# Kernel optimization log

Measured on AMD Instinct MI355X. Metric: run time of the kernel, lower is better.

The kernel has to match this reference:

```python
import jax, jax.numpy as jnp
import numpy as np

D_MODEL = 256
V_OUT = 256
N1 = 8192
N2 = 8192
NUM_CLASSES = 10


def _cross_sup_con_loss(features, labels_y1, labels_y2):
    """Label-masked softmax contrastive loss over a [N1, N2] score matrix.

    mask[i, j] = 1 if labels_y1[i] == labels_y2[j]. Standard SupCon-style
    stabilized log-softmax over dim 1; loss = -mean_i mean_{j in pos(i)} log p_ij.
    Returns (masked softmax probabilities, scalar loss).
    """
    mask = (labels_y1[:, None] == labels_y2[None, :]).astype(features.dtype)  # [N1, N2]
    logits = features - jax.lax.stop_gradient(jnp.max(features, axis=1, keepdims=True))
    log_prob = logits - jax.nn.logsumexp(logits, axis=1, keepdims=True)  # [N1, N2]
    pos_per_row = jnp.maximum(jnp.sum(mask, axis=1), 1.0)
    mean_log_prob_pos = jnp.sum(mask * log_prob, axis=1) / pos_per_row
    loss = -jnp.mean(mean_log_prob_pos)
    masked_prob = mask * jnp.exp(log_prob)
    return masked_prob, loss


def setup_inputs() -> dict:
    key = jax.random.key(0)
    ks = jax.random.split(key, 10)
    s = 1.0 / np.sqrt(D_MODEL)
    inp = {
        "x1": jax.random.normal(ks[0], (N1, D_MODEL), jnp.float32),
        "x2": jax.random.normal(ks[1], (N2, D_MODEL), jnp.float32),
        "labels_y1": jax.random.randint(ks[2], (N1,), 0, NUM_CLASSES, jnp.int64 if jax.config.jax_enable_x64 else jnp.int32),
        "labels_y2": jax.random.randint(ks[3], (N2,), 0, NUM_CLASSES, jnp.int64 if jax.config.jax_enable_x64 else jnp.int32),
        # Linear params stored as [in, out]; y = x @ W + b
        "Wxq": jax.random.normal(ks[4], (D_MODEL, D_MODEL), jnp.float32) * s,
        "bxq": jnp.zeros((D_MODEL,), jnp.float32),
        "Wxk": jax.random.normal(ks[5], (D_MODEL, D_MODEL), jnp.float32) * s,
        "bxk": jnp.zeros((D_MODEL,), jnp.float32),
        "Wxv": jax.random.normal(ks[6], (D_MODEL, V_OUT), jnp.float32) * s,
        "bxv": jnp.zeros((V_OUT,), jnp.float32),
        "Wout": jax.random.normal(ks[7], (V_OUT, V_OUT), jnp.float32) * s,
        "bout": jnp.zeros((V_OUT,), jnp.float32),
    }
    return inp


def reference(x1, x2, labels_y1, labels_y2, Wxq, bxq, Wxk, bxk, Wxv, bxv, Wout, bout):
    scale = 1.0 / jnp.asarray(D_MODEL, x1.dtype) ** 0.5  # self.d_k overwritten to d_model
    x_q = x1 @ Wxq + bxq                 # [N1, D]
    x_k = x2 @ Wxk + bxk                 # [N2, D]
    x_v = x2 @ Wxv + bxv                 # [N2, V]
    scores = (x_q @ x_k.T) * scale       # [N1, N2]
    masked_prob, loss = _cross_sup_con_loss(scores, labels_y1, labels_y2)
    out = masked_prob @ x_v              # [N1, V]
    res = x1 + out                       # residual (d_model == v_out_dim)
    # F.normalize: L2 along dim=1, eps=1e-12
    norm = jnp.linalg.norm(res, axis=1, keepdims=True)
    res = res / jnp.maximum(norm, 1e-12)
    output = jax.nn.relu(res @ Wout + bout)
    return loss, output
```

## Files before the change

### kernel.cpp

```cpp
#include <hip/hip_runtime.h>
#include <math.h>

#define DM 256
#define NROWS 8192
#define NCOLS 8192
#define LOG2E 1.44269504f
#define LN2F 0.6931471805599453f

typedef __attribute__((ext_vector_type(8)))  __bf16 bf16x8;
typedef __attribute__((ext_vector_type(4)))  __bf16 bf16x4;
typedef __attribute__((ext_vector_type(16))) float  f32x16;

#if __has_builtin(__builtin_amdgcn_exp2f)
#define EXP2F(x) __builtin_amdgcn_exp2f(x)
#else
#define EXP2F(x) exp2f(x)
#endif

__device__ __forceinline__ f32x16 fzero16() {
  f32x16 z;
#pragma unroll
  for (int i = 0; i < 16; ++i) z[i] = 0.f;
  return z;
}

__device__ __forceinline__ void load_lds16(const void* g, void* l) {
  __builtin_amdgcn_global_load_lds(
      (const __attribute__((address_space(1))) unsigned int*)g,
      (__attribute__((address_space(3))) unsigned int*)l, 16, 0, 0);
}

__device__ __forceinline__ bf16x8 cvt8(float4 a, float4 b) {
  bf16x8 v;
  v[0] = (__bf16)a.x; v[1] = (__bf16)a.y; v[2] = (__bf16)a.z; v[3] = (__bf16)a.w;
  v[4] = (__bf16)b.x; v[5] = (__bf16)b.y; v[6] = (__bf16)b.z; v[7] = (__bf16)b.w;
  return v;
}

__device__ __forceinline__ unsigned cvtpk_bf16(float lo, float hi) {
  unsigned r;
  asm("v_cvt_pk_bf16_f32 %0, %1, %2" : "=v"(r) : "v"(lo), "v"(hi));
  return r;
}
__device__ __forceinline__ void swap32(unsigned& a, unsigned& b) {
  asm("v_permlane32_swap_b32 %0, %1" : "+v"(a), "+v"(b));
}

__global__ __launch_bounds__(256) void convert_w_kernel(
    const float* __restrict__ W0, const float* __restrict__ W1,
    const float* __restrict__ W2, const float* __restrict__ W3,
    __bf16* __restrict__ wt) {
  __shared__ float Ls[64][65];
  const int t = threadIdx.x;
  const int mat = blockIdx.x >> 4;
  const int k0 = ((blockIdx.x >> 2) & 3) * 64;
  const int n0 = (blockIdx.x & 3) * 64;
  const float* W = mat == 0 ? W0 : mat == 1 ? W1 : mat == 2 ? W2 : W3;
#pragma unroll
  for (int i = 0; i < 4; ++i) {
    int idx = t + i * 256;
    int row = idx >> 4, c4 = (idx & 15) * 4;
    float4 v = *(const float4*)&W[(size_t)(k0 + row) * DM + n0 + c4];
    Ls[row][c4] = v.x; Ls[row][c4 + 1] = v.y;
    Ls[row][c4 + 2] = v.z; Ls[row][c4 + 3] = v.w;
  }
  __syncthreads();
#pragma unroll
  for (int i = 0; i < 2; ++i) {
    int c = t + i * 256;
    int n = c >> 3, kc = (c & 7) * 8;
    bf16x8 v;
#pragma unroll
    for (int j = 0; j < 8; ++j) v[j] = (__bf16)Ls[kc + j][n];
    *(bf16x8*)&wt[(size_t)mat * 65536 + (size_t)(n0 + n) * DM + k0 + kc] = v;
  }
}

__global__ __launch_bounds__(1024) void hist_kernel(
    const int* __restrict__ lab2, int* __restrict__ counts) {
  __shared__ int h[16];
  const int t = threadIdx.x;
  if (t < 16) h[t] = 0;
  __syncthreads();
  int4 a = *(const int4*)&lab2[t * 8];
  int4 b = *(const int4*)&lab2[t * 8 + 4];
  atomicAdd(&h[a.x & 15], 1); atomicAdd(&h[a.y & 15], 1);
  atomicAdd(&h[a.z & 15], 1); atomicAdd(&h[a.w & 15], 1);
  atomicAdd(&h[b.x & 15], 1); atomicAdd(&h[b.y & 15], 1);
  atomicAdd(&h[b.z & 15], 1); atomicAdd(&h[b.w & 15], 1);
  __syncthreads();
  if (t < 16) counts[t] = h[t];
}

__global__ __launch_bounds__(256) void proj3_kernel(
    const float* __restrict__ x1, const float* __restrict__ x2,
    const __bf16* __restrict__ wt, const float* __restrict__ bxq,
    const float* __restrict__ bxk, const float* __restrict__ bxv,
    __bf16* __restrict__ xqb, __bf16* __restrict__ xkb,
    __bf16* __restrict__ xvT) {
  __shared__ __bf16 W_s[64 * 256];
  const int t = threadIdx.x;
  const int w = t >> 6, l = t & 63, g = l >> 5, l31 = l & 31;
  const int mb = blockIdx.x, nt = blockIdx.y, mat = blockIdx.z;
  const int n0 = nt * 64;
  const float* A = (mat == 0) ? x1 : x2;
  const __bf16* wmat = wt + (size_t)mat * 65536;
  const float* bias = (mat == 0) ? bxq : (mat == 1) ? bxk : bxv;
  const float oscale = (mat == 0) ? (0.0625f * LOG2E) : 1.0f;
#pragma unroll
  for (int o = 0; o < 8; ++o) {
    int cbase = w * 64 + o * 256;
    int chunk = cbase + l;
    int n = chunk >> 5, kb = (chunk & 31) * 16;
    load_lds16((const char*)wmat + (size_t)(n0 + n) * 512 + (kb ^ ((n & 7) << 4)),
               (char*)W_s + (size_t)cbase * 16);
  }
  const int arow = mb * 128 + w * 32 + l31;
  bf16x8 af[16];
#pragma unroll
  for (int ks = 0; ks < 16; ++ks) {
    float4 u0 = *(const float4*)&A[(size_t)arow * DM + ks * 16 + g * 8];
    float4 u1 = *(const float4*)&A[(size_t)arow * DM + ks * 16 + g * 8 + 4];
    af[ks] = cvt8(u0, u1);
  }
  __syncthreads();
  f32x16 acc2[2];
  acc2[0] = fzero16(); acc2[1] = fzero16();
#pragma unroll
  for (int ks = 0; ks < 16; ++ks)
#pragma unroll
    for (int tt = 0; tt < 2; ++tt) {
      int n = tt * 32 + l31;
      bf16x8 b = *(const bf16x8*)&W_s[n * DM + ((ks * 16 + g * 8) ^ ((n & 7) << 3))];
      acc2[tt] = __builtin_amdgcn_mfma_f32_32x32x16_bf16(af[ks], b, acc2[tt], 0, 0, 0);
    }
  const int mrowbase = mb * 128 + w * 32;
#pragma unroll
  for (int tt = 0; tt < 2; ++tt) {
    const int col = n0 + tt * 32 + l31;
    const float bv = bias[col];
    if (mat == 2) {
#pragma unroll
      for (int rq = 0; rq < 4; ++rq) {
        int m = mrowbase + 8 * rq + 4 * g;
        bf16x4 v;
#pragma unroll
        for (int j = 0; j < 4; ++j) v[j] = (__bf16)(acc2[tt][rq * 4 + j] + bv);
        *(bf16x4*)&xvT[(size_t)col * NROWS + m] = v;
      }
    } else {
      __bf16* dst = (mat == 0) ? xqb : xkb;
#pragma unroll
      for (int rq = 0; rq < 4; ++rq)
#pragma unroll
        for (int j = 0; j < 4; ++j) {
          int m = mrowbase + j + 8 * rq + 4 * g;
          dst[(size_t)m * DM + col] = (__bf16)((acc2[tt][rq * 4 + j] + bv) * oscale);
        }
    }
  }
}

__device__ __forceinline__ void stage_tiles32(
    const __bf16* __restrict__ xkb, const __bf16* __restrict__ xvT,
    __bf16* Kbuf, __bf16* Vbuf, int j0, int w, int l) {
#pragma unroll
  for (int o = 0; o < 4; ++o) {
    int cbase = o * 256 + w * 64;
    int c = cbase + l;
    int j = c >> 5, kg = (c & 31) * 16;
    load_lds16((const char*)xkb + (size_t)(j0 + j) * 512 + (kg ^ ((j & 7) << 4)),
               (char*)Kbuf + (size_t)cbase * 16);
  }
#pragma unroll
  for (int o = 0; o < 4; ++o) {
    int cbase = o * 256 + w * 64;
    int c = cbase + l;
    int p = c ^ ((c >> 3) & 7);
    int v = p >> 2, jg = p & 3;
    load_lds16((const char*)xvT + (size_t)v * 16384 + (size_t)j0 * 2 + jg * 16,
               (char*)Vbuf + (size_t)cbase * 16);
  }
}

__global__ __launch_bounds__(256, 2) void flash_kernel(
    const __bf16* __restrict__ xqb, const __bf16* __restrict__ xkb,
    const __bf16* __restrict__ xvT, const int* __restrict__ lab1,
    const int* __restrict__ lab2, __bf16* __restrict__ accp,
    float* __restrict__ sgp, float* __restrict__ psp) {
  __shared__ __align__(16) char smem[66560];
  __bf16* K_s0 = (__bf16*)smem;
  __bf16* VT_s0 = (__bf16*)(smem + 32768);
  unsigned* lpk = (unsigned*)(smem + 65536);

  const int t = threadIdx.x;
  const int w = t >> 6, l = t & 63, g = l >> 5, l31 = l & 31;
  const int qh = w >> 1, vh = w & 1;
  const int f = blockIdx.x;
  const int js = f & 7;
  const int qb = f >> 3;
  const int j0base = js * 1024;

  {
    int4 lv = *(const int4*)&lab2[j0base + t * 4];
    lpk[t] = (unsigned)(lv.x & 255) | ((unsigned)(lv.y & 255) << 8) |
             ((unsigned)(lv.z & 255) << 16) | ((unsigned)(lv.w & 255) << 24);
  }

  const int qrow = qb * 64 + qh * 32 + l31;
  bf16x8 qf[16];
#pragma unroll
  for (int ks = 0; ks < 16; ++ks)
    qf[ks] = *(const bf16x8*)&xqb[(size_t)qrow * DM + ks * 16 + g * 8];
  const unsigned lax = (unsigned)(lab1[qrow] & 255) * 0x01010101u;

  float s_p = 0.f, ps_p = 0.f;
  f32x16 acc[4];
#pragma unroll
  for (int tt = 0; tt < 4; ++tt) acc[tt] = fzero16();

  __syncthreads();

  stage_tiles32(xkb, xvT, K_s0, VT_s0, j0base, w, l);
  stage_tiles32(xkb, xvT, K_s0 + 8192, VT_s0 + 8192, j0base + 32, w, l);

  union PaU { unsigned uu[4]; bf16x8 v; };

#pragma unroll 1
  for (int it = 0; it < 32; ++it) {
    if (it < 31) {
      asm volatile("s_waitcnt vmcnt(8)" ::: "memory");
    } else {
      asm volatile("s_waitcnt vmcnt(0)" ::: "memory");
    }
    __builtin_amdgcn_sched_barrier(0);
    __builtin_amdgcn_s_barrier();
    __builtin_amdgcn_sched_barrier(0);

    const __bf16* Kc = K_s0 + (it & 1) * 8192;
    const __bf16* Vc = VT_s0 + (it & 1) * 8192;

    f32x16 c = fzero16();
    __builtin_amdgcn_s_setprio(1);
#pragma unroll
    for (int ks = 0; ks < 16; ++ks) {
      bf16x8 kb = *(const bf16x8*)&Kc[l31 * DM +
                                      ((ks * 16 + g * 8) ^ ((l31 & 7) << 3))];
      c = __builtin_amdgcn_mfma_f32_32x32x16_bf16(kb, qf[ks], c, 0, 0, 0);
    }
    __builtin_amdgcn_s_setprio(0);

    unsigned lb[4];
#pragma unroll
    for (int q4 = 0; q4 < 4; ++q4)
      lb[q4] = lpk[it * 8 + q4 * 2 + g] ^ lax;
#pragma unroll
    for (int r = 0; r < 16; ++r) {
      float sv = c[r];
      float p = EXP2F(sv);
      s_p += p;
      bool mt = ((lb[r >> 2] >> ((r & 3) * 8)) & 255u) == 0u;
      ps_p += mt ? sv : 0.f;
      c[r] = mt ? p : 0.f;
    }
    unsigned u[8];
#pragma unroll
    for (int i = 0; i < 8; ++i) u[i] = cvtpk_bf16(c[2 * i], c[2 * i + 1]);
    swap32(u[0], u[2]); swap32(u[1], u[3]);
    swap32(u[4], u[6]); swap32(u[5], u[7]);
    PaU p0, p1;
    p0.uu[0] = u[0]; p0.uu[1] = u[1]; p0.uu[2] = u[2]; p0.uu[3] = u[3];
    p1.uu[0] = u[4]; p1.uu[1] = u[5]; p1.uu[2] = u[6]; p1.uu[3] = u[7];

    __builtin_amdgcn_s_setprio(1);
#pragma unroll
    for (int tt = 0; tt < 4; ++tt) {
      int v = vh * 128 + tt * 32 + l31;
#pragma unroll
      for (int kj = 0; kj < 2; ++kj) {
        int pg = v * 4 + kj * 2 + g;
        int lg = pg ^ ((pg >> 3) & 7);
        bf16x8 vb = *(const bf16x8*)&Vc[lg * 8];
        acc[tt] = __builtin_amdgcn_mfma_f32_32x32x16_bf16(
            kj ? p1.v : p0.v, vb, acc[tt], 0, 0, 0);
      }
    }
    __builtin_amdgcn_s_setprio(0);

    asm volatile("s_waitcnt lgkmcnt(0)" ::: "memory");
    __builtin_amdgcn_sched_barrier(0);
    __builtin_amdgcn_s_barrier();
    __builtin_amdgcn_sched_barrier(0);
    if (it + 2 < 32)
      stage_tiles32(xkb, xvT, K_s0 + (it & 1) * 8192, VT_s0 + (it & 1) * 8192,
                    j0base + (it + 2) * 32, w, l);
  }

  s_p += __shfl_xor(s_p, 32);
  ps_p += __shfl_xor(ps_p, 32);
  if (vh == 0 && l < 32) {
    sgp[(size_t)js * NROWS + qrow] = s_p;
    psp[(size_t)js * NROWS + qrow] = ps_p;
  }
  __bf16* st = (__bf16*)smem;
#pragma unroll
  for (int tt = 0; tt < 4; ++tt)
#pragma unroll
    for (int r = 0; r < 16; ++r) {
      int row = qh * 32 + (r & 3) + 8 * (r >> 2) + 4 * g;
      int col = vh * 128 + tt * 32 + l31;
      st[row * 264 + col] = (__bf16)acc[tt][r];
    }
  __syncthreads();
  __bf16* dst = accp + ((size_t)js * NROWS + qb * 64) * DM;
#pragma unroll
  for (int p = 0; p < 8; ++p) {
    int off16 = p * 256 + t;
    int row = off16 >> 5;
    int colg = off16 & 31;
    bf16x8 v = *(const bf16x8*)&st[row * 264 + colg * 8];
    *(bf16x8*)&dst[(size_t)row * DM + colg * 8] = v;
  }
}

__global__ __launch_bounds__(1024) void combine_kernel(
    const __bf16* __restrict__ accp, const float* __restrict__ sgp,
    const float* __restrict__ psp, const int* __restrict__ counts,
    const int* __restrict__ lab1, const float* __restrict__ x1,
    __bf16* __restrict__ resn, float* __restrict__ loss_out) {
  __shared__ float lred[16];
  const int t = threadIdx.x;
  const int rr = t >> 6;
  const int r = blockIdx.x * 16 + rr;
  const int l = t & 63;
  float s = 0.f;
#pragma unroll
  for (int js = 0; js < 8; ++js) s += sgp[(size_t)js * NROWS + r];
  const float inv = 1.f / s;
  float a0 = 0.f, a1 = 0.f, a2 = 0.f, a3 = 0.f;
#pragma unroll
  for (int js = 0; js < 8; ++js) {
    bf16x4 v = *(const bf16x4*)&accp[((size_t)js * NROWS + r) * DM + l * 4];
    a0 += (float)v[0]; a1 += (float)v[1]; a2 += (float)v[2]; a3 += (float)v[3];
  }
  float4 x = *(const float4*)&x1[(size_t)r * DM + l * 4];
  float o0 = x.x + a0 * inv, o1 = x.y + a1 * inv;
  float o2 = x.z + a2 * inv, o3 = x.w + a3 * inv;
  float sq = o0 * o0 + o1 * o1 + o2 * o2 + o3 * o3;
#pragma unroll
  for (int m = 1; m < 64; m <<= 1) sq += __shfl_xor(sq, m);
  const float nrm = 1.f / fmaxf(sqrtf(sq), 1e-12f);
  bf16x4 o;
  o[0] = (__bf16)(o0 * nrm); o[1] = (__bf16)(o1 * nrm);
  o[2] = (__bf16)(o2 * nrm); o[3] = (__bf16)(o3 * nrm);
  *(bf16x4*)&resn[(size_t)r * DM + l * 4] = o;
  if (l == 0) {
    float ps = 0.f;
#pragma unroll
    for (int js = 0; js < 8; ++js) ps += psp[(size_t)js * NROWS + r];
    float np = (float)counts[lab1[r] & 15];
    lred[rr] = (ps * LN2F - np * logf(s)) / fmaxf(np, 1.f);
  }
  __syncthreads();
  if (t == 0) {
    float accl = 0.f;
#pragma unroll
    for (int i = 0; i < 16; ++i) accl += lred[i];
    atomicAdd(loss_out, -accl * (1.f / 8192.f));
  }
}

__global__ __launch_bounds__(256) void final_gemm(
    const __bf16* __restrict__ A, const __bf16* __restrict__ wmat,
    const float* __restrict__ bias, float* __restrict__ C) {
  __shared__ __bf16 W_s[64 * 256];
  const int t = threadIdx.x;
  const int w = t >> 6, l = t & 63, g = l >> 5, l31 = l & 31;
  const int mb = blockIdx.x, nt = blockIdx.y;
  const int n0 = nt * 64;
#pragma unroll
  for (int o = 0; o < 8; ++o) {
    int cbase = w * 64 + o * 256;
    int chunk = cbase + l;
    int n = chunk >> 5, kb = (chunk & 31) * 16;
    load_lds16((const char*)wmat + (size_t)(n0 + n) * 512 + (kb ^ ((n & 7) << 4)),
               (char*)W_s + (size_t)cbase * 16);
  }
  const int arow = mb * 128 + w * 32 + l31;
  bf16x8 af[16];
#pragma unroll
  for (int ks = 0; ks < 16; ++ks)
    af[ks] = *(const bf16x8*)&A[(size_t)arow * DM + ks * 16 + g * 8];
  __syncthreads();
  f32x16 acc2[2];
  acc2[0] = fzero16(); acc2[1] = fzero16();
#pragma unroll
  for (int ks = 0; ks < 16; ++ks)
#pragma unroll
    for (int tt = 0; tt < 2; ++tt) {
      int n = tt * 32 + l31;
      bf16x8 b = *(const bf16x8*)&W_s[n * DM + ((ks * 16 + g * 8) ^ ((n & 7) << 3))];
      acc2[tt] = __builtin_amdgcn_mfma_f32_32x32x16_bf16(af[ks], b, acc2[tt], 0, 0, 0);
    }
  const int mrowbase = mb * 128 + w * 32;
#pragma unroll
  for (int tt = 0; tt < 2; ++tt) {
    const int col = n0 + tt * 32 + l31;
    const float bv = bias[col];
#pragma unroll
    for (int rq = 0; rq < 4; ++rq)
#pragma unroll
      for (int j = 0; j < 4; ++j) {
        int m = mrowbase + j + 8 * rq + 4 * g;
        C[(size_t)m * DM + col] = fmaxf(acc2[tt][rq * 4 + j] + bv, 0.f);
      }
  }
}

extern "C" void kernel_launch(void* const* d_in, const int* in_sizes, int n_in,
                              void* d_out, int out_size, void* d_ws, size_t ws_size,
                              hipStream_t stream) {
  const float* x1 = (const float*)d_in[0];
  const float* x2 = (const float*)d_in[1];
  const int* lab1 = (const int*)d_in[2];
  const int* lab2 = (const int*)d_in[3];
  const float* Wxq = (const float*)d_in[4];
  const float* bxq = (const float*)d_in[5];
  const float* Wxk = (const float*)d_in[6];
  const float* bxk = (const float*)d_in[7];
  const float* Wxv = (const float*)d_in[8];
  const float* bxv = (const float*)d_in[9];
  const float* Wout = (const float*)d_in[10];
  const float* bout = (const float*)d_in[11];
  float* out = (float*)d_out;

  char* ws = (char*)d_ws;
  __bf16* xqb = (__bf16*)ws;
  __bf16* xkb = (__bf16*)(ws + (4 << 20));
  __bf16* xvT = (__bf16*)(ws + (8 << 20));
  __bf16* wt  = (__bf16*)(ws + (12 << 20));
  int* counts = (int*)(ws + (12 << 20) + (512 << 10));
  __bf16* accp = (__bf16*)(ws + (13 << 20));
  float* sgp  = (float*)(ws + (45 << 20));
  float* psp  = (float*)(ws + (45 << 20) + (256 << 10));
  __bf16* resn = xqb;

  hipMemsetAsync(d_out, 0, sizeof(float), stream);

  convert_w_kernel<<<dim3(64), dim3(256), 0, stream>>>(Wxq, Wxk, Wxv, Wout, wt);
  hist_kernel<<<dim3(1), dim3(1024), 0, stream>>>(lab2, counts);

  proj3_kernel<<<dim3(64, 4, 3), dim3(256), 0, stream>>>(
      x1, x2, wt, bxq, bxk, bxv, xqb, xkb, xvT);

  flash_kernel<<<dim3(1024), dim3(256), 0, stream>>>(
      xqb, xkb, xvT, lab1, lab2, accp, sgp, psp);

  combine_kernel<<<dim3(512), dim3(1024), 0, stream>>>(
      accp, sgp, psp, counts, lab1, x1, resn, out);

  final_gemm<<<dim3(64, 4), dim3(256), 0, stream>>>(resn, wt + 196608, bout,
                                                    out + 1);
}
```

Baseline: 172.8 us.

## Software-pipeline QK^T of the next tile with PV of the current tile

Splits K and V staging into separate async loads and computes the score MFMAs for tile it+1 while tile it runs softmax masking and its PV MFMAs. K for tile it+2 is issued right after the top barrier, and V after the bottom barrier, with vmcnt thresholds adjusted to match. The aim is to give the scheduler independent MFMA chains to interleave and to hide the QK^T dependency latency ahead of the exp and pack work. The cost is an extra 16-register score accumulator live across the loop body, which raises register pressure and could hurt occupancy.

```diff
diff --git a/kernel.cpp b/kernel.cpp
--- a/kernel.cpp
+++ b/kernel.cpp
@@ -161,9 +161,8 @@
   }
 }
 
-__device__ __forceinline__ void stage_tiles32(
-    const __bf16* __restrict__ xkb, const __bf16* __restrict__ xvT,
-    __bf16* Kbuf, __bf16* Vbuf, int j0, int w, int l) {
+__device__ __forceinline__ void stage_K32(
+    const __bf16* __restrict__ xkb, __bf16* Kbuf, int j0, int w, int l) {
 #pragma unroll
   for (int o = 0; o < 4; ++o) {
     int cbase = o * 256 + w * 64;
@@ -172,6 +171,9 @@
     load_lds16((const char*)xkb + (size_t)(j0 + j) * 512 + (kg ^ ((j & 7) << 4)),
                (char*)Kbuf + (size_t)cbase * 16);
   }
+}
+__device__ __forceinline__ void stage_V32(
+    const __bf16* __restrict__ xvT, __bf16* Vbuf, int j0, int w, int l) {
 #pragma unroll
   for (int o = 0; o < 4; ++o) {
     int cbase = o * 256 + w * 64;
@@ -221,35 +223,42 @@
 
   __syncthreads();
 
-  stage_tiles32(xkb, xvT, K_s0, VT_s0, j0base, w, l);
-  stage_tiles32(xkb, xvT, K_s0 + 8192, VT_s0 + 8192, j0base + 32, w, l);
+  stage_K32(xkb, K_s0, j0base, w, l);
+  stage_V32(xvT, VT_s0, j0base, w, l);
+  stage_K32(xkb, K_s0 + 8192, j0base + 32, w, l);
+  stage_V32(xvT, VT_s0 + 8192, j0base + 32, w, l);
+
+  asm volatile("s_waitcnt vmcnt(8)" ::: "memory");
+  __builtin_amdgcn_sched_barrier(0);
+  __builtin_amdgcn_s_barrier();
+  __builtin_amdgcn_sched_barrier(0);
+
+  f32x16 c = fzero16();
+  __builtin_amdgcn_s_setprio(1);
+#pragma unroll
+  for (int ks = 0; ks < 16; ++ks) {
+    bf16x8 kb = *(const bf16x8*)&K_s0[l31 * DM +
+                                      ((ks * 16 + g * 8) ^ ((l31 & 7) << 3))];
+    c = __builtin_amdgcn_mfma_f32_32x32x16_bf16(kb, qf[ks], c, 0, 0, 0);
+  }
+  __builtin_amdgcn_s_setprio(0);
 
   union PaU { unsigned uu[4]; bf16x8 v; };
 
 #pragma unroll 1
   for (int it = 0; it < 32; ++it) {
     if (it < 31) {
-      asm volatile("s_waitcnt vmcnt(8)" ::: "memory");
+      asm volatile("s_waitcnt vmcnt(4)" ::: "memory");
     } else {
       asm volatile("s_waitcnt vmcnt(0)" ::: "memory");
     }
     __builtin_amdgcn_sched_barrier(0);
     __builtin_amdgcn_s_barrier();
     __builtin_amdgcn_sched_barrier(0);
-
-    const __bf16* Kc = K_s0 + (it & 1) * 8192;
-    const __bf16* Vc = VT_s0 + (it & 1) * 8192;
-
-    f32x16 c = fzero16();
+    if (it + 2 < 32)
+      stage_K32(xkb, K_s0 + (it & 1) * 8192, j0base + (it + 2) * 32, w, l);
+
     __builtin_amdgcn_s_setprio(1);
-#pragma unroll
-    for (int ks = 0; ks < 16; ++ks) {
-      bf16x8 kb = *(const bf16x8*)&Kc[l31 * DM +
-                                      ((ks * 16 + g * 8) ^ ((l31 & 7) << 3))];
-      c = __builtin_amdgcn_mfma_f32_32x32x16_bf16(kb, qf[ks], c, 0, 0, 0);
-    }
-    __builtin_amdgcn_s_setprio(0);
-
     unsigned lb[4];
 #pragma unroll
     for (int q4 = 0; q4 < 4; ++q4)
@@ -272,7 +281,18 @@
     p0.uu[0] = u[0]; p0.uu[1] = u[1]; p0.uu[2] = u[2]; p0.uu[3] = u[3];
     p1.uu[0] = u[4]; p1.uu[1] = u[5]; p1.uu[2] = u[6]; p1.uu[3] = u[7];
 
-    __builtin_amdgcn_s_setprio(1);
+    f32x16 cn = fzero16();
+    if (it < 31) {
+      const __bf16* Kn = K_s0 + ((it + 1) & 1) * 8192;
+#pragma unroll
+      for (int ks = 0; ks < 16; ++ks) {
+        bf16x8 kb = *(const bf16x8*)&Kn[l31 * DM +
+                                        ((ks * 16 + g * 8) ^ ((l31 & 7) << 3))];
+        cn = __builtin_amdgcn_mfma_f32_32x32x16_bf16(kb, qf[ks], cn, 0, 0, 0);
+      }
+    }
+
+    const __bf16* Vc = VT_s0 + (it & 1) * 8192;
 #pragma unroll
     for (int tt = 0; tt < 4; ++tt) {
       int v = vh * 128 + tt * 32 + l31;
@@ -292,8 +312,9 @@
     __builtin_amdgcn_s_barrier();
     __builtin_amdgcn_sched_barrier(0);
     if (it + 2 < 32)
-      stage_tiles32(xkb, xvT, K_s0 + (it & 1) * 8192, VT_s0 + (it & 1) * 8192,
-                    j0base + (it + 2) * 32, w, l);
+      stage_V32(xvT, VT_s0 + (it & 1) * 8192, j0base + (it + 2) * 32, w, l);
+
+    c = cn;
   }
 
   s_p += __shfl_xor(s_p, 32);
```

Measured after the change: 185.9 us. 7.5% more time.

## Split softmax exp work between wave pairs and exchange P fragments via LDS

Applied to the files above, without the earlier changes.

Each pair of waves sharing the same query rows previously computed the full exp/mask/convert on all 16 score elements redundantly. Now each wave handles half the elements, writes its packed bf16 P fragment to a new LDS exchange buffer, synchronizes, and reads the partner's half. Row sums are combined across the pair through LDS at the end. This halves transcendental and mask work per wave but adds an extra block barrier and LDS round-trip per iteration, plus more shared memory that could affect occupancy.

```diff
diff --git a/kernel.cpp b/kernel.cpp
--- a/kernel.cpp
+++ b/kernel.cpp
@@ -188,10 +188,11 @@
     const __bf16* __restrict__ xvT, const int* __restrict__ lab1,
     const int* __restrict__ lab2, __bf16* __restrict__ accp,
     float* __restrict__ sgp, float* __restrict__ psp) {
-  __shared__ __align__(16) char smem[66560];
+  __shared__ __align__(16) char smem[70656];
   __bf16* K_s0 = (__bf16*)smem;
   __bf16* VT_s0 = (__bf16*)(smem + 32768);
   unsigned* lpk = (unsigned*)(smem + 65536);
+  uint4* Pex = (uint4*)(smem + 66560);
 
   const int t = threadIdx.x;
   const int w = t >> 6, l = t & 63, g = l >> 5, l31 = l & 31;
@@ -250,27 +251,39 @@
     }
     __builtin_amdgcn_s_setprio(0);
 
-    unsigned lb[4];
-#pragma unroll
-    for (int q4 = 0; q4 < 4; ++q4)
-      lb[q4] = lpk[it * 8 + q4 * 2 + g] ^ lax;
-#pragma unroll
-    for (int r = 0; r < 16; ++r) {
+    const int rb = vh * 8;
+    unsigned lb[2];
+#pragma unroll
+    for (int h = 0; h < 2; ++h)
+      lb[h] = lpk[it * 8 + (vh * 2 + h) * 2 + g] ^ lax;
+#pragma unroll
+    for (int rr = 0; rr < 8; ++rr) {
+      int r = rb + rr;
       float sv = c[r];
       float p = EXP2F(sv);
       s_p += p;
-      bool mt = ((lb[r >> 2] >> ((r & 3) * 8)) & 255u) == 0u;
+      bool mt = ((lb[rr >> 2] >> ((rr & 3) * 8)) & 255u) == 0u;
       ps_p += mt ? sv : 0.f;
       c[r] = mt ? p : 0.f;
     }
-    unsigned u[8];
-#pragma unroll
-    for (int i = 0; i < 8; ++i) u[i] = cvtpk_bf16(c[2 * i], c[2 * i + 1]);
+    unsigned u[4];
+#pragma unroll
+    for (int i = 0; i < 4; ++i)
+      u[i] = cvtpk_bf16(c[rb + 2 * i], c[rb + 2 * i + 1]);
     swap32(u[0], u[2]); swap32(u[1], u[3]);
-    swap32(u[4], u[6]); swap32(u[5], u[7]);
+    uint4 own;
+    own.x = u[0]; own.y = u[1]; own.z = u[2]; own.w = u[3];
+    Pex[w * 64 + l] = own;
+    asm volatile("s_waitcnt lgkmcnt(0)" ::: "memory");
+    __builtin_amdgcn_sched_barrier(0);
+    __builtin_amdgcn_s_barrier();
+    __builtin_amdgcn_sched_barrier(0);
+    uint4 oth = Pex[(w ^ 1) * 64 + l];
     PaU p0, p1;
-    p0.uu[0] = u[0]; p0.uu[1] = u[1]; p0.uu[2] = u[2]; p0.uu[3] = u[3];
-    p1.uu[0] = u[4]; p1.uu[1] = u[5]; p1.uu[2] = u[6]; p1.uu[3] = u[7];
+    p0.uu[0] = vh ? oth.x : own.x; p0.uu[1] = vh ? oth.y : own.y;
+    p0.uu[2] = vh ? oth.z : own.z; p0.uu[3] = vh ? oth.w : own.w;
+    p1.uu[0] = vh ? own.x : oth.x; p1.uu[1] = vh ? own.y : oth.y;
+    p1.uu[2] = vh ? own.z : oth.z; p1.uu[3] = vh ? own.w : oth.w;
 
     __builtin_amdgcn_s_setprio(1);
 #pragma unroll
@@ -298,9 +311,17 @@
 
   s_p += __shfl_xor(s_p, 32);
   ps_p += __shfl_xor(ps_p, 32);
+  float* sred = (float*)(smem + 66560);
+  if (l < 32) {
+    sred[(w * 32 + l31) * 2] = s_p;
+    sred[(w * 32 + l31) * 2 + 1] = ps_p;
+  }
+  __syncthreads();
   if (vh == 0 && l < 32) {
-    sgp[(size_t)js * NROWS + qrow] = s_p;
-    psp[(size_t)js * NROWS + qrow] = ps_p;
+    float stot = s_p + sred[((w ^ 1) * 32 + l31) * 2];
+    float ptot = ps_p + sred[((w ^ 1) * 32 + l31) * 2 + 1];
+    sgp[(size_t)js * NROWS + qrow] = stot;
+    psp[(size_t)js * NROWS + qrow] = ptot;
   }
   __bf16* st = (__bf16*)smem;
 #pragma unroll
```

New measurement: 331.1 us. 1.92x slower.

## Fuse weight conversion, histogram and loss memset into one prep kernel; split row-sum work

Applied to the files above, without the earlier changes.

Merges the weight-conversion kernel, the label histogram kernel and the loss memset into a single prep kernel launch with an extra block, cutting two launches. In the flash kernel, each wave half now accumulates the softmax denominator and positive-logit sums only for its own share of rows instead of redundantly over all rows, and partial sums are combined across wave pairs through shared memory. The reduction adds one extra __syncthreads and some shared-memory traffic at the kernel tail.

```diff
diff --git a/kernel.cpp b/kernel.cpp
--- a/kernel.cpp
+++ b/kernel.cpp
@@ -46,12 +46,28 @@
   asm("v_permlane32_swap_b32 %0, %1" : "+v"(a), "+v"(b));
 }
 
-__global__ __launch_bounds__(256) void convert_w_kernel(
+__global__ __launch_bounds__(256) void prep_kernel(
     const float* __restrict__ W0, const float* __restrict__ W1,
     const float* __restrict__ W2, const float* __restrict__ W3,
-    __bf16* __restrict__ wt) {
+    __bf16* __restrict__ wt, const int* __restrict__ lab2,
+    int* __restrict__ counts, float* __restrict__ loss_out) {
+  const int t = threadIdx.x;
+  if (blockIdx.x == 64) {
+    __shared__ int h[16];
+    if (t < 16) h[t] = 0;
+    __syncthreads();
+#pragma unroll
+    for (int i = 0; i < 8; ++i) {
+      int4 a = *(const int4*)&lab2[t * 32 + i * 4];
+      atomicAdd(&h[a.x & 15], 1); atomicAdd(&h[a.y & 15], 1);
+      atomicAdd(&h[a.z & 15], 1); atomicAdd(&h[a.w & 15], 1);
+    }
+    __syncthreads();
+    if (t < 16) counts[t] = h[t];
+    if (t == 0) *loss_out = 0.f;
+    return;
+  }
   __shared__ float Ls[64][65];
-  const int t = threadIdx.x;
   const int mat = blockIdx.x >> 4;
   const int k0 = ((blockIdx.x >> 2) & 3) * 64;
   const int n0 = (blockIdx.x & 3) * 64;
@@ -74,22 +90,6 @@
     for (int j = 0; j < 8; ++j) v[j] = (__bf16)Ls[kc + j][n];
     *(bf16x8*)&wt[(size_t)mat * 65536 + (size_t)(n0 + n) * DM + k0 + kc] = v;
   }
-}
-
-__global__ __launch_bounds__(1024) void hist_kernel(
-    const int* __restrict__ lab2, int* __restrict__ counts) {
-  __shared__ int h[16];
-  const int t = threadIdx.x;
-  if (t < 16) h[t] = 0;
-  __syncthreads();
-  int4 a = *(const int4*)&lab2[t * 8];
-  int4 b = *(const int4*)&lab2[t * 8 + 4];
-  atomicAdd(&h[a.x & 15], 1); atomicAdd(&h[a.y & 15], 1);
-  atomicAdd(&h[a.z & 15], 1); atomicAdd(&h[a.w & 15], 1);
-  atomicAdd(&h[b.x & 15], 1); atomicAdd(&h[b.y & 15], 1);
-  atomicAdd(&h[b.z & 15], 1); atomicAdd(&h[b.w & 15], 1);
-  __syncthreads();
-  if (t < 16) counts[t] = h[t];
 }
 
 __global__ __launch_bounds__(256) void proj3_kernel(
@@ -258,9 +258,11 @@
     for (int r = 0; r < 16; ++r) {
       float sv = c[r];
       float p = EXP2F(sv);
-      s_p += p;
       bool mt = ((lb[r >> 2] >> ((r & 3) * 8)) & 255u) == 0u;
-      ps_p += mt ? sv : 0.f;
+      if ((r >> 3) == vh) {
+        s_p += p;
+        ps_p += mt ? sv : 0.f;
+      }
       c[r] = mt ? p : 0.f;
     }
     unsigned u[8];
@@ -298,9 +300,17 @@
 
   s_p += __shfl_xor(s_p, 32);
   ps_p += __shfl_xor(ps_p, 32);
+  float* sred = (float*)(smem + 65536);
+  if (l < 32) {
+    sred[(w * 32 + l31) * 2] = s_p;
+    sred[(w * 32 + l31) * 2 + 1] = ps_p;
+  }
+  __syncthreads();
   if (vh == 0 && l < 32) {
-    sgp[(size_t)js * NROWS + qrow] = s_p;
-    psp[(size_t)js * NROWS + qrow] = ps_p;
+    float stot = s_p + sred[(((w ^ 1) * 32) + l31) * 2];
+    float ptot = ps_p + sred[(((w ^ 1) * 32) + l31) * 2 + 1];
+    sgp[(size_t)js * NROWS + qrow] = stot;
+    psp[(size_t)js * NROWS + qrow] = ptot;
   }
   __bf16* st = (__bf16*)smem;
 #pragma unroll
@@ -445,10 +455,8 @@
   float* psp  = (float*)(ws + (45 << 20) + (256 << 10));
   __bf16* resn = xqb;
 
-  hipMemsetAsync(d_out, 0, sizeof(float), stream);
-
-  convert_w_kernel<<<dim3(64), dim3(256), 0, stream>>>(Wxq, Wxk, Wxv, Wout, wt);
-  hist_kernel<<<dim3(1), dim3(1024), 0, stream>>>(lab2, counts);
+  prep_kernel<<<dim3(65), dim3(256), 0, stream>>>(Wxq, Wxk, Wxv, Wout, wt,
+                                                  lab2, counts, out);
 
   proj3_kernel<<<dim3(64, 4, 3), dim3(256), 0, stream>>>(
       x1, x2, wt, bxq, bxk, bxv, xqb, xkb, xvT);
```

Result: faster. 167.6 us (-3.0%).
